# Kernel tuning notes

Hardware: AMD Instinct MI355X
Metric: run time of the kernel (lower is better)

The kernel has to match this reference:

```python
import jax, jax.numpy as jnp
import numpy as np

T, D, O, L, R = 8192, 4096, 4096, 8, 16  # tokens, in_dim, out_dim, max_loras, lora_rank


def setup_inputs() -> dict:
    key = jax.random.key(0)
    k0, k1, k2, k3, k4 = jax.random.split(key, 5)
    x = jax.random.normal(k0, (T, D), dtype=jnp.float32)
    weight = jax.random.normal(k1, (O, D), dtype=jnp.float32) * 0.02   # base Linear weight
    lora_a = jax.random.normal(k2, (L, R, D), dtype=jnp.float32) * 0.02  # stacked A (slice dim squeezed)
    lora_b = jax.random.normal(k3, (L, O, R), dtype=jnp.float32) * 0.02  # stacked B
    token_lora_idx = jax.random.randint(k4, (T,), 0, L, dtype=jnp.int32)  # per-token adapter id
    return {"x": x, "weight": weight, "lora_a": lora_a, "lora_b": lora_b,
            "token_lora_idx": token_lora_idx}


def reference(x, weight, lora_a, lora_b, token_lora_idx):
    # base linear (no bias)
    base = jnp.einsum('td,od->to', x, weight)
    # punica add_lora_linear, single slice, scale = 1.0:
    # per-token gather of A/B expressed as a one-hot contraction (small L, rank R)
    onehot = jax.nn.one_hot(token_lora_idx, lora_a.shape[0], dtype=x.dtype)  # [T, L]
    shrink = jnp.einsum('td,lrd->tlr', x, lora_a)          # [T, L, R] (tiny: R=16)
    s = jnp.einsum('tlr,tl->tr', shrink, onehot)           # select this token's adapter
    delta = jnp.einsum('tr,lor,tl->to', s, lora_b, onehot) # expand + scatter-add
    return base + delta
```

## Files before the change

kernel.cpp:

```cpp
#include <hip/hip_runtime.h>
#include <hip/hip_bf16.h>
#include <stdint.h>

#define T_TOK 8192
#define DIM 4096
#define ODIM 4096
#define NL 8
#define RANK 16
#define KAUG 4224
#define NKT (KAUG / 64)

__device__ __forceinline__ uint16_t f2b(float x) {
    uint32_t u = __builtin_bit_cast(uint32_t, x);
    u += 0x7fffu + ((u >> 16) & 1u);
    return (uint16_t)(u >> 16);
}

typedef __attribute__((ext_vector_type(4))) float floatx4;
typedef __attribute__((ext_vector_type(8))) __bf16 bf16x8;

__device__ __forceinline__ void load_lds16(const uint16_t* g, uint16_t* l) {
    __builtin_amdgcn_global_load_lds(
        (const __attribute__((address_space(1))) uint32_t*)g,
        (__attribute__((address_space(3))) uint32_t*)l, 16, 0, 0);
}

__global__ __launch_bounds__(256) void pack_all(const float* __restrict__ x,
                                                const float* __restrict__ W,
                                                const float* __restrict__ la,
                                                const float* __restrict__ lb,
                                                uint16_t* __restrict__ xaug,
                                                uint16_t* __restrict__ waug,
                                                uint16_t* __restrict__ aall) {
    int b = blockIdx.x;
    int tid = threadIdx.x;
    const float* src;
    uint16_t* dst;
    if (b < ODIM)               { src = W  + (size_t)b * DIM;                 dst = waug + (size_t)b * KAUG; }
    else if (b < ODIM + T_TOK)  { int t = b - ODIM;
                                  src = x  + (size_t)t * DIM;                 dst = xaug + (size_t)t * KAUG; }
    else                        { int r = b - ODIM - T_TOK;
                                  src = la + (size_t)r * DIM;                 dst = aall + (size_t)r * DIM; }
#pragma unroll
    for (int k = 0; k < 4; ++k) {
        int i4 = k * 256 + tid;
        float4 v = ((const float4*)src)[i4];
        ushort4 bv;
        bv.x = f2b(v.x); bv.y = f2b(v.y); bv.z = f2b(v.z); bv.w = f2b(v.w);
        *(ushort4*)(dst + (size_t)i4 * 4) = bv;
    }
    if (b < ODIM && tid < NL * RANK) {
        int l = tid >> 4, r = tid & 15;
        dst[DIM + tid] = f2b(lb[((size_t)l * ODIM + b) * RANK + r]);
    }
}

#define SBM 32
__global__ __launch_bounds__(256) void shrink_gemm(const uint16_t* __restrict__ xa,
                                                   const uint16_t* __restrict__ aall,
                                                   const int* __restrict__ idx,
                                                   uint16_t* __restrict__ xaug) {
    __shared__ uint16_t sA[SBM * 64];
    __shared__ uint16_t sB[128 * 64];
    int tid = threadIdx.x, lane = tid & 63, wid = tid >> 6;
    int bm = blockIdx.x;
    int q = lane >> 4, r16 = lane & 15;

    int rS = tid >> 3;
    int kcS = (tid & 7) ^ (rS & 7);
    const uint16_t* gA = xa + (size_t)(bm * SBM + rS) * KAUG + kcS * 8;
    const uint16_t* gB0 = aall + (size_t)(rS) * DIM + kcS * 8;
    const uint16_t* gB1 = aall + (size_t)(32 + rS) * DIM + kcS * 8;
    const uint16_t* gB2 = aall + (size_t)(64 + rS) * DIM + kcS * 8;
    const uint16_t* gB3 = aall + (size_t)(96 + rS) * DIM + kcS * 8;
    uint16_t* lA  = sA + wid * 512;
    uint16_t* lB0 = sB + wid * 512;
    uint16_t* lB1 = sB + 2048 + wid * 512;
    uint16_t* lB2 = sB + 4096 + wid * 512;
    uint16_t* lB3 = sB + 6144 + wid * 512;

    int sw0 = (q ^ (r16 & 7)) * 8;
    int sw1 = ((4 + q) ^ (r16 & 7)) * 8;

    floatx4 acc[2][2];
#pragma unroll
    for (int i = 0; i < 2; ++i)
#pragma unroll
        for (int j = 0; j < 2; ++j) acc[i][j] = (floatx4){0.f, 0.f, 0.f, 0.f};

    for (int k0 = 0; k0 < DIM; k0 += 64) {
        __syncthreads();
        load_lds16(gA + k0, lA);
        load_lds16(gB0 + k0, lB0);
        load_lds16(gB1 + k0, lB1);
        load_lds16(gB2 + k0, lB2);
        load_lds16(gB3 + k0, lB3);
        __syncthreads();
#pragma unroll
        for (int kk = 0; kk < 2; ++kk) {
            int sw = kk ? sw1 : sw0;
            bf16x8 af[2], bv[2];
#pragma unroll
            for (int i = 0; i < 2; ++i)
                af[i] = *(const bf16x8*)(sA + (i * 16 + r16) * 64 + sw);
#pragma unroll
            for (int j = 0; j < 2; ++j)
                bv[j] = *(const bf16x8*)(sB + (wid * 32 + j * 16 + r16) * 64 + sw);
#pragma unroll
            for (int i = 0; i < 2; ++i)
#pragma unroll
                for (int j = 0; j < 2; ++j)
                    acc[i][j] = __builtin_amdgcn_mfma_f32_16x16x32_bf16(af[i], bv[j], acc[i][j], 0, 0, 0);
        }
    }
#pragma unroll
    for (int i = 0; i < 2; ++i) {
#pragma unroll
        for (int j = 0; j < 2; ++j) {
            int p = wid * 32 + j * 16 + r16;
            int lp = p >> 4;
#pragma unroll
            for (int e = 0; e < 4; ++e) {
                int t = bm * SBM + i * 16 + q * 4 + e;
                uint16_t v = (idx[t] == lp) ? f2b(acc[i][j][e]) : (uint16_t)0;
                xaug[(size_t)t * KAUG + DIM + p] = v;
            }
        }
    }
}

#define GBM 256
#define GBN 256

__global__ __launch_bounds__(512) void gemm_aug8(const uint16_t* __restrict__ A,
                                                 const uint16_t* __restrict__ B,
                                                 float* __restrict__ C) {
    __shared__ uint16_t sA[2][GBM * 64];
    __shared__ uint16_t sB[2][GBN * 64];

    int tid = threadIdx.x;
    int lane = tid & 63, wid = tid >> 6;
    int q = lane >> 4, r16 = lane & 15;
    int wm = (wid >> 2) * 128;
    int wn = (wid & 3) * 64;

    int cpx = gridDim.x >> 3;
    int wgid = (blockIdx.x & 7) * cpx + (blockIdx.x >> 3);
    int bn = wgid & 15;
    int bm = wgid >> 4;

    int rS = tid >> 3;
    int cS = (tid & 7) ^ (rS & 7);
    const uint16_t* gA0 = A + (size_t)(bm * GBM + rS) * KAUG + cS * 8;
    const uint16_t* gB0 = B + (size_t)(bn * GBN + rS) * KAUG + cS * 8;
    int ldsOff = wid * 512;

    auto stageA = [&](int bufi, int half, int tk) {
        const uint16_t* g = gA0 + (size_t)(half * 128) * KAUG + (size_t)tk * 64;
        uint16_t* l = &sA[bufi][half * 8192 + ldsOff];
        load_lds16(g, l);
        load_lds16(g + (size_t)64 * KAUG, l + 4096);
    };
    auto stageB = [&](int bufi, int half, int tk) {
        const uint16_t* g = gB0 + (size_t)(half * 128) * KAUG + (size_t)tk * 64;
        uint16_t* l = &sB[bufi][half * 8192 + ldsOff];
        load_lds16(g, l);
        load_lds16(g + (size_t)64 * KAUG, l + 4096);
    };

    int swz[2] = { ((0 + q) ^ (r16 & 7)) * 8, ((4 + q) ^ (r16 & 7)) * 8 };

    bf16x8 aH[4][2];
    bf16x8 bfv[4][2];
    floatx4 acc[8][4];
#pragma unroll
    for (int i = 0; i < 8; ++i)
#pragma unroll
        for (int j = 0; j < 4; ++j) acc[i][j] = (floatx4){0.f, 0.f, 0.f, 0.f};

    auto rdA = [&](int b, int mh) {
#pragma unroll
        for (int mf = 0; mf < 4; ++mf)
#pragma unroll
            for (int kk = 0; kk < 2; ++kk)
                aH[mf][kk] = *(const bf16x8*)&sA[b][(wm + mh * 64 + mf * 16 + r16) * 64 + swz[kk]];
    };
    auto rdB = [&](int b) {
#pragma unroll
        for (int nf = 0; nf < 4; ++nf)
#pragma unroll
            for (int kk = 0; kk < 2; ++kk)
                bfv[nf][kk] = *(const bf16x8*)&sB[b][(wn + nf * 16 + r16) * 64 + swz[kk]];
    };
    auto mmaQ = [&](int mh, int nh) {
        __builtin_amdgcn_s_setprio(1);
#pragma unroll
        for (int mf = 0; mf < 4; ++mf)
#pragma unroll
            for (int nf = 0; nf < 2; ++nf)
#pragma unroll
                for (int kk = 0; kk < 2; ++kk)
                    acc[mh * 4 + mf][nh * 2 + nf] = __builtin_amdgcn_mfma_f32_16x16x32_bf16(
                        aH[mf][kk], bfv[nh * 2 + nf][kk], acc[mh * 4 + mf][nh * 2 + nf], 0, 0, 0);
        __builtin_amdgcn_s_setprio(0);
    };

#define BAR  __builtin_amdgcn_s_barrier()
#define LGK0 { asm volatile("s_waitcnt lgkmcnt(0)" ::: "memory"); __builtin_amdgcn_sched_barrier(0); }
#define VM6  asm volatile("s_waitcnt vmcnt(6)" ::: "memory")
#define VM0  asm volatile("s_waitcnt vmcnt(0)" ::: "memory")

    stageB(0, 0, 0); stageB(0, 1, 0); stageA(0, 0, 0); stageA(0, 1, 0);
    stageB(1, 0, 1); stageB(1, 1, 1); stageA(1, 0, 1);
    VM6;
    BAR;

#pragma unroll 1
    for (int i = 0; i < NKT / 2; ++i) {
        int t1 = 2 * i + 1, t2 = 2 * i + 2, t3 = 2 * i + 3;
        rdB(0); rdA(0, 0);
        stageA(1, 1, t1);
        BAR; LGK0; mmaQ(0, 0); BAR;
        if (t2 < NKT) stageB(0, 0, t2);
        BAR; mmaQ(0, 1); BAR;
        rdA(0, 1);
        if (t2 < NKT) stageB(0, 1, t2);
        BAR; LGK0; mmaQ(1, 0); BAR;
        if (t2 < NKT) { stageA(0, 0, t2); VM6; } else { VM0; }
        BAR; mmaQ(1, 1); BAR;
        rdB(1); rdA(1, 0);
        if (t2 < NKT) stageA(0, 1, t2);
        BAR; LGK0; mmaQ(0, 0); BAR;
        if (t3 < NKT) stageB(1, 0, t3);
        BAR; mmaQ(0, 1); BAR;
        rdA(1, 1);
        if (t3 < NKT) stageB(1, 1, t3);
        BAR; LGK0; mmaQ(1, 0); BAR;
        if (t3 < NKT) { stageA(1, 0, t3); VM6; } else { VM0; }
        BAR; mmaQ(1, 1); BAR;
    }

#pragma unroll
    for (int mf = 0; mf < 8; ++mf) {
#pragma unroll
        for (int nf = 0; nf < 4; ++nf) {
            int col = bn * GBN + wn + nf * 16 + r16;
            int rowb = bm * GBM + wm + mf * 16 + q * 4;
#pragma unroll
            for (int e = 0; e < 4; ++e)
                C[(size_t)(rowb + e) * ODIM + col] = acc[mf][nf][e];
        }
    }
#undef BAR
#undef LGK0
#undef VM6
#undef VM0
}

extern "C" void kernel_launch(void* const* d_in, const int* in_sizes, int n_in,
                              void* d_out, int out_size, void* d_ws, size_t ws_size,
                              hipStream_t stream) {
    const float* x  = (const float*)d_in[0];
    const float* W  = (const float*)d_in[1];
    const float* la = (const float*)d_in[2];
    const float* lb = (const float*)d_in[3];
    const int* idx  = (const int*)d_in[4];
    float* out = (float*)d_out;

    uint16_t* xaug = (uint16_t*)d_ws;
    uint16_t* waug = xaug + (size_t)T_TOK * KAUG;
    uint16_t* aall = waug + (size_t)ODIM * KAUG;

    hipLaunchKernelGGL(pack_all, dim3(ODIM + T_TOK + NL * RANK), dim3(256), 0, stream,
                       x, W, la, lb, xaug, waug, aall);
    hipLaunchKernelGGL(shrink_gemm, dim3(T_TOK / SBM), dim3(256), 0, stream,
                       xaug, aall, idx, xaug);
    hipLaunchKernelGGL(gemm_aug8, dim3((T_TOK / GBM) * (ODIM / GBN)), dim3(512), 0, stream,
                       xaug, waug, out);
}
```

Baseline: 551.4 us.

## Restructure GEMM main loop pipeline with interleaved A/B staging and fewer barriers

Reworks the double-buffered global-to-LDS pipeline of the augmented bf16 GEMM. A tiles are now staged in interleaved row parts rather than halves, and B fragments are read per N-half just before use. Explicit lgkmcnt waits and about half of the barriers are removed in favour of vmcnt-based waits, so LDS reads, async loads and MFMA can overlap more. The cost is correctness that now depends on the tighter wait/barrier ordering, which risks LDS read/write hazards.

```diff
diff --git a/kernel.cpp b/kernel.cpp
--- a/kernel.cpp
+++ b/kernel.cpp
@@ -155,13 +155,13 @@
     const uint16_t* gB0 = B + (size_t)(bn * GBN + rS) * KAUG + cS * 8;
     int ldsOff = wid * 512;
 
-    auto stageA = [&](int bufi, int half, int tk) {
-        const uint16_t* g = gA0 + (size_t)(half * 128) * KAUG + (size_t)tk * 64;
-        uint16_t* l = &sA[bufi][half * 8192 + ldsOff];
-        load_lds16(g, l);
-        load_lds16(g + (size_t)64 * KAUG, l + 4096);
-    };
-    auto stageB = [&](int bufi, int half, int tk) {
+    auto stageA2 = [&](int bufi, int part, int tk) {
+        const uint16_t* g = gA0 + (size_t)tk * 64;
+        uint16_t* l = &sA[bufi][ldsOff];
+        load_lds16(g + (size_t)(part * 64) * KAUG,       l + part * 4096);
+        load_lds16(g + (size_t)((part + 2) * 64) * KAUG, l + (part + 2) * 4096);
+    };
+    auto stageBh = [&](int bufi, int half, int tk) {
         const uint16_t* g = gB0 + (size_t)(half * 128) * KAUG + (size_t)tk * 64;
         uint16_t* l = &sB[bufi][half * 8192 + ldsOff];
         load_lds16(g, l);
@@ -185,12 +185,12 @@
             for (int kk = 0; kk < 2; ++kk)
                 aH[mf][kk] = *(const bf16x8*)&sA[b][(wm + mh * 64 + mf * 16 + r16) * 64 + swz[kk]];
     };
-    auto rdB = [&](int b) {
-#pragma unroll
-        for (int nf = 0; nf < 4; ++nf)
+    auto rdBq = [&](int b, int nh) {
+#pragma unroll
+        for (int nf = 0; nf < 2; ++nf)
 #pragma unroll
             for (int kk = 0; kk < 2; ++kk)
-                bfv[nf][kk] = *(const bf16x8*)&sB[b][(wn + nf * 16 + r16) * 64 + swz[kk]];
+                bfv[nh * 2 + nf][kk] = *(const bf16x8*)&sB[b][(wn + (nh * 2 + nf) * 16 + r16) * 64 + swz[kk]];
     };
     auto mmaQ = [&](int mh, int nh) {
         __builtin_amdgcn_s_setprio(1);
@@ -206,38 +206,51 @@
     };
 
 #define BAR  __builtin_amdgcn_s_barrier()
-#define LGK0 { asm volatile("s_waitcnt lgkmcnt(0)" ::: "memory"); __builtin_amdgcn_sched_barrier(0); }
 #define VM6  asm volatile("s_waitcnt vmcnt(6)" ::: "memory")
+#define VM8  asm volatile("s_waitcnt vmcnt(8)" ::: "memory")
 #define VM0  asm volatile("s_waitcnt vmcnt(0)" ::: "memory")
 
-    stageB(0, 0, 0); stageB(0, 1, 0); stageA(0, 0, 0); stageA(0, 1, 0);
-    stageB(1, 0, 1); stageB(1, 1, 1); stageA(1, 0, 1);
-    VM6;
-    BAR;
+    stageA2(0, 0, 0); stageBh(0, 0, 0); stageBh(0, 1, 0); stageA2(0, 1, 0);
+    stageA2(1, 0, 1); stageBh(1, 0, 1);
 
 #pragma unroll 1
     for (int i = 0; i < NKT / 2; ++i) {
         int t1 = 2 * i + 1, t2 = 2 * i + 2, t3 = 2 * i + 3;
-        rdB(0); rdA(0, 0);
-        stageA(1, 1, t1);
-        BAR; LGK0; mmaQ(0, 0); BAR;
-        if (t2 < NKT) stageB(0, 0, t2);
-        BAR; mmaQ(0, 1); BAR;
+        bool full = (t2 < NKT);
+
+        VM6; BAR;
+        rdA(0, 0); rdBq(0, 0);
+        stageBh(1, 1, t1);
+        mmaQ(0, 0);
+        BAR;
+        rdBq(0, 1);
+        stageA2(1, 1, t1);
+        mmaQ(0, 1);
+        VM8; BAR;
         rdA(0, 1);
-        if (t2 < NKT) stageB(0, 1, t2);
-        BAR; LGK0; mmaQ(1, 0); BAR;
-        if (t2 < NKT) { stageA(0, 0, t2); VM6; } else { VM0; }
-        BAR; mmaQ(1, 1); BAR;
-        rdB(1); rdA(1, 0);
-        if (t2 < NKT) stageA(0, 1, t2);
-        BAR; LGK0; mmaQ(0, 0); BAR;
-        if (t3 < NKT) stageB(1, 0, t3);
-        BAR; mmaQ(0, 1); BAR;
+        if (full) stageA2(0, 0, t2);
+        mmaQ(1, 0);
+        BAR;
+        if (full) stageBh(0, 0, t2);
+        mmaQ(1, 1);
+
+        if (full) { VM6; } else { VM0; }
+        BAR;
+        rdA(1, 0); rdBq(1, 0);
+        if (full) stageBh(0, 1, t2);
+        mmaQ(0, 0);
+        BAR;
+        rdBq(1, 1);
+        if (full) stageA2(0, 1, t2);
+        mmaQ(0, 1);
+        if (full) { VM8; } else { VM0; }
+        BAR;
         rdA(1, 1);
-        if (t3 < NKT) stageB(1, 1, t3);
-        BAR; LGK0; mmaQ(1, 0); BAR;
-        if (t3 < NKT) { stageA(1, 0, t3); VM6; } else { VM0; }
-        BAR; mmaQ(1, 1); BAR;
+        if (t3 < NKT) stageA2(1, 0, t3);
+        mmaQ(1, 0);
+        BAR;
+        if (t3 < NKT) stageBh(1, 0, t3);
+        mmaQ(1, 1);
     }
 
 #pragma unroll
@@ -252,8 +265,8 @@
         }
     }
 #undef BAR
-#undef LGK0
 #undef VM6
+#undef VM8
 #undef VM0
 }
 
```

After: 551.3 us. Within noise of the previous version (-0.0%).
